# Kernel tuning notes

Measured on AMD Instinct MI355X. Metric: run time of the kernel, lower is better.

## Reference

```python
import jax, jax.numpy as jnp
import numpy as np

EPS = 1e-5
FH, FW, OC = 1, 9, 32  # filt_h, filt_w, out_channels (hardcoded in HypER)


def _bn(x, g, b, axes):
    # training-mode batchnorm: biased variance over `axes`
    m = jnp.mean(x, axis=axes, keepdims=True)
    v = jnp.mean(jnp.square(x - m), axis=axes, keepdims=True)
    return (x - m) * jax.lax.rsqrt(v + EPS) * g + b


def setup_inputs() -> dict:
    key = jax.random.key(0)
    ks = jax.random.split(key, 8)
    N, INPUT_D, D1, D2, B = 50000, 400, 400, 400, 8192
    fc_len = OC * (D1 - FW + 1)  # 32*392 = 12544
    return {
        "head_tail_id": jax.random.randint(ks[0], (2, B), 0, N, dtype=jnp.int32),
        "unique_entity_embed": jax.random.normal(ks[1], (N, INPUT_D), jnp.float32),
        "W_E": jax.random.normal(ks[2], (INPUT_D, D1), jnp.float32) * 0.05,
        "fc1_w": jax.random.normal(ks[3], (OC * FW, D2), jnp.float32) * 0.05,
        "fc1_b": jnp.zeros((OC * FW,), jnp.float32),
        "fc_w": jax.random.normal(ks[4], (D1, fc_len), jnp.float32) * 0.02,
        "fc_b": jnp.zeros((D1,), jnp.float32),
        "bn0_g": jnp.ones((1,), jnp.float32),
        "bn0_b": jnp.zeros((1,), jnp.float32),
        "bn1_g": jnp.ones((OC,), jnp.float32),
        "bn1_b": jnp.zeros((OC,), jnp.float32),
        "bn2_g": jnp.ones((400,), jnp.float32),
        "bn2_b": jnp.zeros((400,), jnp.float32),
    }


def reference(head_tail_id, unique_entity_embed, W_E, fc1_w, fc1_b, fc_w, fc_b,
              bn0_g, bn0_b, bn1_g, bn1_b, bn2_g, bn2_b):
    E = unique_entity_embed @ W_E                    # (N, d1)
    head = E[head_tail_id[0]]                        # (B, d1)
    tail = E[head_tail_id[1]]                        # (B, d1)
    # bn0: BatchNorm2d with 1 channel -> normalize over all B*1*d1 elements
    x = _bn(head, bn0_g[0], bn0_b[0], axes=(0, 1))   # (B, d1)
    # hypernetwork: per-sample dynamic 1x9 filters for 32 out-channels
    k = (tail @ fc1_w.T + fc1_b).reshape(-1, OC, FW)  # (B, 32, 9)
    W_out = x.shape[1] - FW + 1                       # d1-8 = 392
    win_idx = jnp.arange(W_out)[:, None] + jnp.arange(FW)[None, :]
    xw = x[:, win_idx]                                # (B, W_out, 9) sliding windows
    # grouped conv (groups=B), cross-correlation as in F.conv2d
    conv = jnp.einsum('bjw,bow->boj', xw, k)          # (B, 32, W_out)
    # bn1: per out-channel over (B, W_out)
    conv = _bn(conv, bn1_g[None, :, None], bn1_b[None, :, None], axes=(0, 2))
    feat = conv.reshape(conv.shape[0], -1)            # (B, 32*W_out), channel-major flatten
    out = feat @ fc_w.T + fc_b                        # (B, d1)
    out = _bn(out, bn2_g, bn2_b, axes=(0,))           # BatchNorm1d over batch
    return jax.nn.relu(out)
```

## Files before the change

kernel.cpp:

```cpp
#include <hip/hip_runtime.h>


#define BB   8192
#define DD   400
#define RR   288
#define OCC  32
#define FWW  9
#define JJ   392
#define FCLEN 12544
#define KSPL 4
#define KS   (FCLEN / KSPL)
#define KSTEPS (KS / 64)
#define EPSF 1e-5
#define RB2  512

typedef __attribute__((ext_vector_type(8))) short bf16x8;
typedef __attribute__((ext_vector_type(4))) float f32x4;

__device__ inline unsigned short f2bf(float f) {
    union { float f; unsigned u; } x; x.f = f;
    unsigned r = x.u + 0x7fffu + ((x.u >> 16) & 1u);
    return (unsigned short)(r >> 16);
}

__device__ inline void gload16(const void* g, void* l) {
    __builtin_amdgcn_global_load_lds((const __attribute__((address_space(1))) unsigned int*)g,
                                     (__attribute__((address_space(3))) unsigned int*)l, 16, 0, 0);
}

__device__ inline float block_reduce_256(float v, float* red) {
    #pragma unroll
    for (int m = 1; m < 64; m <<= 1) v += __shfl_xor(v, m);
    int wv = threadIdx.x >> 6;
    if ((threadIdx.x & 63) == 0) red[wv] = v;
    __syncthreads();
    float r = 0.f;
    if (threadIdx.x == 0) r = red[0] + red[1] + red[2] + red[3];
    return r;
}

__global__ __launch_bounds__(256) void prep_M(const float* __restrict__ WE,
                                              const float* __restrict__ f1w,
                                              float* __restrict__ Mout) {
    __shared__ float sA[16][17];
    __shared__ float sB[16][17];
    int tx = threadIdx.x, ty = threadIdx.y;
    int r0 = blockIdx.x * 16, i0 = blockIdx.y * 16;
    float acc = 0.f;
    for (int d0 = 0; d0 < DD; d0 += 16) {
        sA[ty][tx] = WE[(size_t)(i0 + ty) * DD + d0 + tx];
        sB[ty][tx] = f1w[(size_t)(r0 + ty) * DD + d0 + tx];
        __syncthreads();
        #pragma unroll
        for (int dd = 0; dd < 16; ++dd) acc = fmaf(sA[ty][dd], sB[tx][dd], acc);
        __syncthreads();
    }
    Mout[(size_t)(i0 + ty) * RR + r0 + tx] = acc;
}

template <int BN>
__global__ __launch_bounds__(256) void gemm_s1(const float* __restrict__ A,
                                               const int* __restrict__ idx,
                                               const float* __restrict__ Bm,
                                               const float* __restrict__ bias,
                                               float* __restrict__ C, int N,
                                               float* __restrict__ bn0part) {
    constexpr int BNF = BN / 16;
    constexpr int BCH = 64 * (BN / 4) / 256;
    __shared__ unsigned short Al[64][72];
    __shared__ unsigned short Bl[BN][72];
    __shared__ int ridx[64];
    __shared__ float red[8];
    int tid = threadIdx.x;
    int bm = blockIdx.x, bn = blockIdx.y;
    if (tid < 64) ridx[tid] = idx[bm * 64 + tid];
    int lane = tid & 63, wv = tid >> 6;
    int m16 = lane & 15, kb = lane >> 4;
    f32x4 acc[BNF];
    #pragma unroll
    for (int nb = 0; nb < BNF; ++nb) acc[nb] = (f32x4){0.f, 0.f, 0.f, 0.f};
    __syncthreads();

    float4 av[4];
    float4 bv[BCH];
    auto LOADR = [&](int k0) {
        #pragma unroll
        for (int r = 0; r < 4; ++r) {
            int c = tid + 256 * r;
            int row = c >> 4, kq = c & 15;
            int gk = k0 + kq * 4;
            av[r] = (float4){0.f, 0.f, 0.f, 0.f};
            if (gk < DD) av[r] = *(const float4*)(A + (size_t)ridx[row] * DD + gk);
        }
        #pragma unroll
        for (int r = 0; r < BCH; ++r) {
            int c = tid + 256 * r;
            int kk2 = c / (BN / 4), nq = c % (BN / 4);
            int gk = k0 + kk2;
            bv[r] = (float4){0.f, 0.f, 0.f, 0.f};
            if (gk < DD) bv[r] = *(const float4*)(Bm + (size_t)gk * N + bn * BN + nq * 4);
        }
    };
    auto WRITELDS = [&]() {
        #pragma unroll
        for (int r = 0; r < 4; ++r) {
            int c = tid + 256 * r;
            int row = c >> 4, kq = c & 15;
            ushort4 p;
            p.x = f2bf(av[r].x); p.y = f2bf(av[r].y); p.z = f2bf(av[r].z); p.w = f2bf(av[r].w);
            *(ushort4*)&Al[row][kq * 4] = p;
        }
        #pragma unroll
        for (int r = 0; r < BCH; ++r) {
            int c = tid + 256 * r;
            int kk2 = c / (BN / 4), nq = c % (BN / 4);
            Bl[nq * 4 + 0][kk2] = f2bf(bv[r].x);
            Bl[nq * 4 + 1][kk2] = f2bf(bv[r].y);
            Bl[nq * 4 + 2][kk2] = f2bf(bv[r].z);
            Bl[nq * 4 + 3][kk2] = f2bf(bv[r].w);
        }
    };

    LOADR(0);
    for (int kt = 0; kt < 7; ++kt) {
        WRITELDS();
        __syncthreads();
        if (kt + 1 < 7) LOADR((kt + 1) * 64);
        #pragma unroll
        for (int ks = 0; ks < 2; ++ks) {
            bf16x8 a = *(const bf16x8*)&Al[wv * 16 + m16][ks * 32 + kb * 8];
            #pragma unroll
            for (int nb = 0; nb < BNF; ++nb) {
                bf16x8 b = *(const bf16x8*)&Bl[nb * 16 + m16][ks * 32 + kb * 8];
                acc[nb] = __builtin_amdgcn_mfma_f32_16x16x32_bf16(a, b, acc[nb], 0, 0, 0);
            }
        }
        __syncthreads();
    }
    float s1 = 0.f, s2 = 0.f;
    #pragma unroll
    for (int nb = 0; nb < BNF; ++nb)
        #pragma unroll
        for (int rr = 0; rr < 4; ++rr) {
            int gr = bm * 64 + wv * 16 + kb * 4 + rr;
            int gc = bn * BN + nb * 16 + m16;
            float v = acc[nb][rr];
            if (bias) v += bias[gc];
            C[(size_t)gr * N + gc] = v;
            s1 += v; s2 = fmaf(v, v, s2);
        }
    if (bn0part) {
        float t1 = block_reduce_256(s1, red);
        __syncthreads();
        float t2 = block_reduce_256(s2, red);
        if (tid == 0) {
            int pid = bm * gridDim.y + bn;
            bn0part[pid * 2] = t1; bn0part[pid * 2 + 1] = t2;
        }
    }
}

__global__ __launch_bounds__(256) void bn0_fin(const float* __restrict__ part,
                                               const float* __restrict__ g,
                                               const float* __restrict__ b,
                                               float* __restrict__ ab0) {
    __shared__ float red[8];
    float s1 = 0.f, s2 = 0.f;
    for (int i = threadIdx.x; i < 640; i += 256) {
        s1 += part[i * 2]; s2 += part[i * 2 + 1];
    }
    float t1 = block_reduce_256(s1, red);
    __syncthreads();
    float t2 = block_reduce_256(s2, red);
    if (threadIdx.x == 0) {
        double n = (double)BB * DD;
        double mean = (double)t1 / n;
        double var = (double)t2 / n - mean * mean;
        float a0 = (float)((double)g[0] / sqrt(var + EPSF));
        float b0 = (float)((double)b[0] - mean * a0);
        ab0[0] = a0; ab0[1] = b0;
    }
}

__global__ __launch_bounds__(256) void conv_k(const float* __restrict__ head,
                                              const float* __restrict__ kbuf,
                                              const float* __restrict__ ab0,
                                              unsigned short* __restrict__ convb,
                                              float* __restrict__ chpartT) {
    __shared__ float xs[DD];
    __shared__ float ks[RR];
    int b = blockIdx.x, tid = threadIdx.x;
    float a0 = ab0[0], b0 = ab0[1];
    for (int i = tid; i < DD; i += 256) xs[i] = fmaf(head[(size_t)b * DD + i], a0, b0);
    for (int i = tid; i < RR; i += 256) ks[i] = kbuf[(size_t)b * RR + i];
    __syncthreads();
    int lane = tid & 63, wv = tid >> 6;
    unsigned short* orow = convb + (size_t)b * FCLEN;
    float kk[8][FWW];
    #pragma unroll
    for (int oi = 0; oi < 8; ++oi)
        #pragma unroll
        for (int w2 = 0; w2 < FWW; ++w2) kk[oi][w2] = ks[(wv * 8 + oi) * FWW + w2];
    float s1[8], s2[8];
    #pragma unroll
    for (int oi = 0; oi < 8; ++oi) { s1[oi] = 0.f; s2[oi] = 0.f; }
    #pragma unroll
    for (int jt = 0; jt < 2; ++jt) {
        int j0 = jt * 256 + lane * 4;
        if (j0 < JJ) {
            const float4* x4 = (const float4*)xs;
            float4 va = x4[(j0 >> 2)], vb = x4[(j0 >> 2) + 1], vc = x4[(j0 >> 2) + 2];
            float x[12] = {va.x, va.y, va.z, va.w, vb.x, vb.y, vb.z, vb.w, vc.x, vc.y, vc.z, vc.w};
            #pragma unroll
            for (int oi = 0; oi < 8; ++oi) {
                float acc[4];
                #pragma unroll
                for (int q = 0; q < 4; ++q) {
                    float a = 0.f;
                    #pragma unroll
                    for (int w2 = 0; w2 < FWW; ++w2) a = fmaf(x[q + w2], kk[oi][w2], a);
                    acc[q] = a;
                }
                ushort4 p;
                p.x = f2bf(acc[0]); p.y = f2bf(acc[1]); p.z = f2bf(acc[2]); p.w = f2bf(acc[3]);
                *(ushort4*)(orow + (wv * 8 + oi) * JJ + j0) = p;
                #pragma unroll
                for (int q = 0; q < 4; ++q) { s1[oi] += acc[q]; s2[oi] = fmaf(acc[q], acc[q], s2[oi]); }
            }
        }
    }
    #pragma unroll
    for (int oi = 0; oi < 8; ++oi) {
        float a = s1[oi], c = s2[oi];
        #pragma unroll
        for (int m = 1; m < 64; m <<= 1) { a += __shfl_xor(a, m); c += __shfl_xor(c, m); }
        if (lane == 0) {
            int o = wv * 8 + oi;
            chpartT[(size_t)o * BB + b] = a;
            chpartT[(size_t)(OCC + o) * BB + b] = c;
        }
    }
}

__global__ __launch_bounds__(256) void bn1_fin(const float* __restrict__ chpartT,
                                               const float* __restrict__ g1,
                                               const float* __restrict__ b1,
                                               float* __restrict__ alphabeta) {
    __shared__ float red[8];
    int o = blockIdx.x, tid = threadIdx.x;
    float s1 = 0.f, s2 = 0.f;
    for (int t = tid; t < BB; t += 256) {
        s1 += chpartT[(size_t)o * BB + t];
        s2 += chpartT[(size_t)(OCC + o) * BB + t];
    }
    float t1 = block_reduce_256(s1, red);
    __syncthreads();
    float t2 = block_reduce_256(s2, red);
    if (tid == 0) {
        double n = (double)BB * JJ;
        double mean = (double)t1 / n;
        double var = (double)t2 / n - mean * mean;
        float al = (float)((double)g1[o] / sqrt(var + EPSF));
        float be = (float)((double)b1[o] - mean * al);
        alphabeta[o] = al; alphabeta[OCC + o] = be;
    }
}

__global__ __launch_bounds__(256) void prep_fcw(const float* __restrict__ fc_w,
                                                const float* __restrict__ fc_b,
                                                const float* __restrict__ alphabeta,
                                                unsigned short* __restrict__ Bp,
                                                float* __restrict__ bias2) {
    __shared__ float al[OCC], be[OCC];
    __shared__ float red[8];
    int d = blockIdx.x, tid = threadIdx.x;
    if (tid < OCC) { al[tid] = alphabeta[tid]; be[tid] = alphabeta[OCC + tid]; }
    __syncthreads();
    const float* row = fc_w + (size_t)d * FCLEN;
    unsigned short* orow = Bp + (size_t)d * FCLEN;
    float bacc = 0.f;
    for (int o = 0; o < OCC; ++o) {
        float a = al[o], bb = be[o];
        for (int j = tid; j < JJ; j += 256) {
            float wv = row[o * JJ + j];
            orow[o * JJ + j] = f2bf(wv * a);
            bacc = fmaf(wv, bb, bacc);
        }
    }
    float t = block_reduce_256(bacc, red);
    if (tid == 0) bias2[d] = fc_b[d] + t;
}

__global__ __launch_bounds__(256, 3) void fc_gemm_sk(const unsigned short* __restrict__ A,
                                                     const unsigned short* __restrict__ Bp,
                                                     float* __restrict__ P) {
    __shared__ __align__(16) unsigned short Al[256 * 64];
    __shared__ __align__(16) unsigned short Bl[80 * 64];
    int tid = threadIdx.x;
    int orig = blockIdx.x;
    int wgid = (orig & 7) * 80 + (orig >> 3);
    int bn = wgid % 5;
    int rest = wgid / 5;
    int bm = rest & 31;
    int bz = rest >> 5;
    int lane = tid & 63, wv = tid >> 6;
    int m16 = lane & 15, kb = lane >> 4;
    int srow = lane >> 3, scol = lane & 7;
    int sw = m16 & 7;
    f32x4 acc[4][5];
    #pragma unroll
    for (int mi = 0; mi < 4; ++mi)
        #pragma unroll
        for (int nb = 0; nb < 5; ++nb) acc[mi][nb] = (f32x4){0.f, 0.f, 0.f, 0.f};

    const unsigned short* Asrc = A + (size_t)(bm * 256 + srow) * FCLEN
                                   + (size_t)bz * KS + ((scol ^ srow) << 3);
    const unsigned short* Bsrc = Bp + (size_t)(bn * 80 + srow) * FCLEN
                                   + (size_t)bz * KS + ((scol ^ srow) << 3);

    for (int kt = 0; kt < KSTEPS; ++kt) {
        const size_t koff = (size_t)kt * 64;
        #pragma unroll
        for (int i = 0; i < 11; ++i) {
            int c = wv + i * 4;
            if (c < 32) {
                gload16(Asrc + (size_t)c * 8 * FCLEN + koff, Al + c * 512);
            } else if (c < 42) {
                int cb = c - 32;
                gload16(Bsrc + (size_t)cb * 8 * FCLEN + koff, Bl + cb * 512);
            }
        }
        __syncthreads();
        #pragma unroll
        for (int ks2 = 0; ks2 < 2; ++ks2) {
            int ch = (((ks2 * 4 + kb) ^ sw) << 3);
            bf16x8 a[4];
            #pragma unroll
            for (int mi = 0; mi < 4; ++mi)
                a[mi] = *(const bf16x8*)(Al + (wv * 64 + mi * 16 + m16) * 64 + ch);
            #pragma unroll
            for (int nb = 0; nb < 5; ++nb) {
                bf16x8 b = *(const bf16x8*)(Bl + (nb * 16 + m16) * 64 + ch);
                #pragma unroll
                for (int mi = 0; mi < 4; ++mi)
                    acc[mi][nb] = __builtin_amdgcn_mfma_f32_16x16x32_bf16(a[mi], b, acc[mi][nb], 0, 0, 0);
            }
        }
        __syncthreads();
    }

    float* Po = P + (size_t)bz * BB * DD;
    #pragma unroll
    for (int mi = 0; mi < 4; ++mi)
        #pragma unroll
        for (int nb = 0; nb < 5; ++nb)
            #pragma unroll
            for (int rr = 0; rr < 4; ++rr) {
                int gr = bm * 256 + wv * 64 + mi * 16 + kb * 4 + rr;
                int gc = bn * 80 + nb * 16 + m16;
                Po[(size_t)gr * DD + gc] = acc[mi][nb][rr];
            }
}

__global__ __launch_bounds__(256) void reduce_bn2(const float* __restrict__ P,
                                                  const float* __restrict__ bias2,
                                                  float* __restrict__ out,
                                                  float* __restrict__ part) {
    int blk = blockIdx.x, tid = threadIdx.x;
    int r0 = blk * 16;
    const size_t S = (size_t)BB * DD;
    bool hasb = tid < DD - 256;
    float bia = bias2[tid];
    float bib = hasb ? bias2[256 + tid] : 0.f;
    float s1a = 0.f, s2a = 0.f, s1b = 0.f, s2b = 0.f;
    for (int r = 0; r < 16; ++r) {
        size_t base = (size_t)(r0 + r) * DD;
        float v = P[base + tid] + P[S + base + tid] + P[2 * S + base + tid] + P[3 * S + base + tid] + bia;
        out[base + tid] = v;
        s1a += v; s2a = fmaf(v, v, s2a);
        if (hasb) {
            size_t b2i = base + 256 + tid;
            float u = P[b2i] + P[S + b2i] + P[2 * S + b2i] + P[3 * S + b2i] + bib;
            out[b2i] = u;
            s1b += u; s2b = fmaf(u, u, s2b);
        }
    }
    float* p = part + (size_t)blk * (DD * 2);
    p[tid * 2] = s1a; p[tid * 2 + 1] = s2a;
    if (hasb) { p[(256 + tid) * 2] = s1b; p[(256 + tid) * 2 + 1] = s2b; }
}

__global__ __launch_bounds__(128) void bn2_fin(const float* __restrict__ part,
                                               const float* __restrict__ g2,
                                               const float* __restrict__ b2,
                                               float* __restrict__ sc,
                                               float* __restrict__ sh) {
    __shared__ float red[4];
    int col = blockIdx.x, tid = threadIdx.x;
    float s1 = 0.f, s2 = 0.f;
    for (int t = tid; t < RB2; t += 128) {
        s1 += part[(size_t)t * (DD * 2) + col * 2];
        s2 += part[(size_t)t * (DD * 2) + col * 2 + 1];
    }
    #pragma unroll
    for (int m = 1; m < 64; m <<= 1) { s1 += __shfl_xor(s1, m); s2 += __shfl_xor(s2, m); }
    int wv = tid >> 6;
    if ((tid & 63) == 0) { red[wv] = s1; red[2 + wv] = s2; }
    __syncthreads();
    if (tid == 0) {
        double t1 = (double)red[0] + red[1];
        double t2 = (double)red[2] + red[3];
        double mean = t1 / (double)BB;
        double var = t2 / (double)BB - mean * mean;
        float s = (float)((double)g2[col] / sqrt(var + EPSF));
        sc[col] = s;
        sh[col] = (float)((double)b2[col] - mean * s);
    }
}

__global__ __launch_bounds__(256) void final_k(float* __restrict__ out,
                                               const float* __restrict__ sc,
                                               const float* __restrict__ sh) {
    __shared__ float lsc[DD], lsh[DD];
    int tid = threadIdx.x;
    for (int c = tid; c < DD; c += 256) { lsc[c] = sc[c]; lsh[c] = sh[c]; }
    __syncthreads();
    size_t base = (size_t)blockIdx.x * 4 * DD;
    for (int r = 0; r < 4; ++r)
        for (int c = tid; c < DD; c += 256) {
            size_t i = base + (size_t)r * DD + c;
            float v = fmaf(out[i], lsc[c], lsh[c]);
            out[i] = v > 0.f ? v : 0.f;
        }
}

extern "C" void kernel_launch(void* const* d_in, const int* in_sizes, int n_in,
                              void* d_out, int out_size, void* d_ws, size_t ws_size,
                              hipStream_t stream) {
    const int* ht      = (const int*)d_in[0];
    const float* UE    = (const float*)d_in[1];
    const float* W_E   = (const float*)d_in[2];
    const float* fc1_w = (const float*)d_in[3];
    const float* fc1_b = (const float*)d_in[4];
    const float* fc_w  = (const float*)d_in[5];
    const float* fc_b  = (const float*)d_in[6];
    const float* bn0_g = (const float*)d_in[7];
    const float* bn0_b = (const float*)d_in[8];
    const float* bn1_g = (const float*)d_in[9];
    const float* bn1_b = (const float*)d_in[10];
    const float* bn2_g = (const float*)d_in[11];
    const float* bn2_b = (const float*)d_in[12];
    float* out = (float*)d_out;

    char* w = (char*)d_ws;
    unsigned short* convb = (unsigned short*)w; w += (size_t)BB * FCLEN * 2;
    unsigned short* Bprep = (unsigned short*)w; w += (size_t)DD * FCLEN * 2;
    float* chpartT = (float*)w; w += (size_t)2 * OCC * BB * 4;
    float* bn0p = (float*)w;  w += 640 * 2 * 4;
    float* ab0 = (float*)w;   w += 64;
    float* alphabeta = (float*)w; w += 64 * 4;
    float* bias2 = (float*)w; w += DD * 4;
    float* bn2p = (float*)w;  w += (size_t)RB2 * DD * 2 * 4;
    float* bn2sc = (float*)w; w += DD * 4;
    float* bn2sh = (float*)w; w += DD * 4;
    float* P = (float*)w;     w += (size_t)KSPL * BB * DD * 4;
    float* head = P;
    float* kbuf = head + (size_t)BB * DD;
    float* Mbuf = kbuf + (size_t)BB * RR;
    (void)ws_size; (void)in_sizes; (void)n_in; (void)out_size;

    prep_M<<<dim3(RR / 16, DD / 16), dim3(16, 16), 0, stream>>>(W_E, fc1_w, Mbuf);
    gemm_s1<80><<<dim3(BB / 64, DD / 80), 256, 0, stream>>>(UE, ht, W_E, nullptr, head, DD, bn0p);
    gemm_s1<96><<<dim3(BB / 64, RR / 96), 256, 0, stream>>>(UE, ht + BB, Mbuf, fc1_b, kbuf, RR, nullptr);
    bn0_fin<<<1, 256, 0, stream>>>(bn0p, bn0_g, bn0_b, ab0);
    conv_k<<<BB, 256, 0, stream>>>(head, kbuf, ab0, convb, chpartT);
    bn1_fin<<<OCC, 256, 0, stream>>>(chpartT, bn1_g, bn1_b, alphabeta);
    prep_fcw<<<DD, 256, 0, stream>>>(fc_w, fc_b, alphabeta, Bprep, bias2);
    fc_gemm_sk<<<dim3(32 * 5 * KSPL), 256, 0, stream>>>(convb, Bprep, P);
    reduce_bn2<<<RB2, 256, 0, stream>>>(P, bias2, out, bn2p);
    bn2_fin<<<DD, 128, 0, stream>>>(bn2p, bn2_g, bn2_b, bn2sc, bn2sh);
    final_k<<<2048, 256, 0, stream>>>(out, bn2sc, bn2sh);
}
```

Before: 336.1 us.

## Fuse bn0 finalize into conv, nontemporal conv stores, vectorize prep_fcw and final_k

Removes the single-block bn0_fin kernel by having every conv_k block redundantly reduce the 640 bn0 partials and compute the scale and shift itself, applying them to the loaded row in registers. Conv output stores become nontemporal 8-byte stores, prep_fcw is rewritten to read fc_w as float4 and write packed bf16x4, and final_k processes 8 rows per block with float4 accesses. The aim is to save a launch, cut cache pollution from the large conv buffer and raise memory efficiency. The cost is 8192 blocks each re-reading and reducing the partials.

```diff
diff --git a/kernel.cpp b/kernel.cpp
--- a/kernel.cpp
+++ b/kernel.cpp
@@ -1,4 +1,5 @@
 #include <hip/hip_runtime.h>
+#include <string.h>
 
 
 #define BB   8192
@@ -16,6 +17,7 @@
 
 typedef __attribute__((ext_vector_type(8))) short bf16x8;
 typedef __attribute__((ext_vector_type(4))) float f32x4;
+typedef __attribute__((ext_vector_type(2))) unsigned int u32x2;
 
 __device__ inline unsigned short f2bf(float f) {
     union { float f; unsigned u; } x; x.f = f;
@@ -26,6 +28,12 @@
 __device__ inline void gload16(const void* g, void* l) {
     __builtin_amdgcn_global_load_lds((const __attribute__((address_space(1))) unsigned int*)g,
                                      (__attribute__((address_space(3))) unsigned int*)l, 16, 0, 0);
+}
+
+__device__ inline void nt_store8(void* addr, ushort4 v) {
+    u32x2 w;
+    memcpy(&w, &v, 8);
+    __builtin_nontemporal_store(w, (u32x2*)addr);
 }
 
 __device__ inline float block_reduce_256(float v, float* red) {
@@ -160,40 +168,34 @@
     }
 }
 
-__global__ __launch_bounds__(256) void bn0_fin(const float* __restrict__ part,
-                                               const float* __restrict__ g,
-                                               const float* __restrict__ b,
-                                               float* __restrict__ ab0) {
-    __shared__ float red[8];
-    float s1 = 0.f, s2 = 0.f;
-    for (int i = threadIdx.x; i < 640; i += 256) {
-        s1 += part[i * 2]; s2 += part[i * 2 + 1];
-    }
-    float t1 = block_reduce_256(s1, red);
-    __syncthreads();
-    float t2 = block_reduce_256(s2, red);
-    if (threadIdx.x == 0) {
-        double n = (double)BB * DD;
-        double mean = (double)t1 / n;
-        double var = (double)t2 / n - mean * mean;
-        float a0 = (float)((double)g[0] / sqrt(var + EPSF));
-        float b0 = (float)((double)b[0] - mean * a0);
-        ab0[0] = a0; ab0[1] = b0;
-    }
-}
-
 __global__ __launch_bounds__(256) void conv_k(const float* __restrict__ head,
                                               const float* __restrict__ kbuf,
-                                              const float* __restrict__ ab0,
+                                              const float* __restrict__ bn0p,
+                                              const float* __restrict__ g0,
+                                              const float* __restrict__ b0g,
                                               unsigned short* __restrict__ convb,
                                               float* __restrict__ chpartT) {
     __shared__ float xs[DD];
     __shared__ float ks[RR];
+    __shared__ float red[8];
+    __shared__ float ab[2];
     int b = blockIdx.x, tid = threadIdx.x;
-    float a0 = ab0[0], b0 = ab0[1];
-    for (int i = tid; i < DD; i += 256) xs[i] = fmaf(head[(size_t)b * DD + i], a0, b0);
+    for (int i = tid; i < DD; i += 256) xs[i] = head[(size_t)b * DD + i];
     for (int i = tid; i < RR; i += 256) ks[i] = kbuf[(size_t)b * RR + i];
-    __syncthreads();
+    float p1 = 0.f, p2 = 0.f;
+    for (int i = tid; i < 640; i += 256) { p1 += bn0p[i * 2]; p2 += bn0p[i * 2 + 1]; }
+    float t1 = block_reduce_256(p1, red);
+    __syncthreads();
+    float t2 = block_reduce_256(p2, red);
+    if (tid == 0) {
+        double n = (double)BB * DD;
+        double mean = (double)t1 / n;
+        double var = (double)t2 / n - mean * mean;
+        float a0 = (float)((double)g0[0] / sqrt(var + EPSF));
+        ab[0] = a0; ab[1] = (float)((double)b0g[0] - mean * a0);
+    }
+    __syncthreads();
+    float a0 = ab[0], b0 = ab[1];
     int lane = tid & 63, wv = tid >> 6;
     unsigned short* orow = convb + (size_t)b * FCLEN;
     float kk[8][FWW];
@@ -210,7 +212,10 @@
         if (j0 < JJ) {
             const float4* x4 = (const float4*)xs;
             float4 va = x4[(j0 >> 2)], vb = x4[(j0 >> 2) + 1], vc = x4[(j0 >> 2) + 2];
-            float x[12] = {va.x, va.y, va.z, va.w, vb.x, vb.y, vb.z, vb.w, vc.x, vc.y, vc.z, vc.w};
+            float xr[12] = {va.x, va.y, va.z, va.w, vb.x, vb.y, vb.z, vb.w, vc.x, vc.y, vc.z, vc.w};
+            float x[12];
+            #pragma unroll
+            for (int q = 0; q < 12; ++q) x[q] = fmaf(xr[q], a0, b0);
             #pragma unroll
             for (int oi = 0; oi < 8; ++oi) {
                 float acc[4];
@@ -223,7 +228,7 @@
                 }
                 ushort4 p;
                 p.x = f2bf(acc[0]); p.y = f2bf(acc[1]); p.z = f2bf(acc[2]); p.w = f2bf(acc[3]);
-                *(ushort4*)(orow + (wv * 8 + oi) * JJ + j0) = p;
+                nt_store8(orow + (wv * 8 + oi) * JJ + j0, p);
                 #pragma unroll
                 for (int q = 0; q < 4; ++q) { s1[oi] += acc[q]; s2[oi] = fmaf(acc[q], acc[q], s2[oi]); }
             }
@@ -276,16 +281,18 @@
     int d = blockIdx.x, tid = threadIdx.x;
     if (tid < OCC) { al[tid] = alphabeta[tid]; be[tid] = alphabeta[OCC + tid]; }
     __syncthreads();
-    const float* row = fc_w + (size_t)d * FCLEN;
-    unsigned short* orow = Bp + (size_t)d * FCLEN;
+    const float4* row4 = (const float4*)(fc_w + (size_t)d * FCLEN);
+    ushort4* orow4 = (ushort4*)(Bp + (size_t)d * FCLEN);
     float bacc = 0.f;
-    for (int o = 0; o < OCC; ++o) {
+    for (int c = tid; c < FCLEN / 4; c += 256) {
+        float4 v = row4[c];
+        int o = c / (JJ / 4);
         float a = al[o], bb = be[o];
-        for (int j = tid; j < JJ; j += 256) {
-            float wv = row[o * JJ + j];
-            orow[o * JJ + j] = f2bf(wv * a);
-            bacc = fmaf(wv, bb, bacc);
-        }
+        ushort4 p;
+        p.x = f2bf(v.x * a); p.y = f2bf(v.y * a);
+        p.z = f2bf(v.z * a); p.w = f2bf(v.w * a);
+        orow4[c] = p;
+        bacc = fmaf(v.x + v.y + v.z + v.w, bb, bacc);
     }
     float t = block_reduce_256(bacc, red);
     if (tid == 0) bias2[d] = fc_b[d] + t;
@@ -425,13 +432,18 @@
     int tid = threadIdx.x;
     for (int c = tid; c < DD; c += 256) { lsc[c] = sc[c]; lsh[c] = sh[c]; }
     __syncthreads();
-    size_t base = (size_t)blockIdx.x * 4 * DD;
-    for (int r = 0; r < 4; ++r)
-        for (int c = tid; c < DD; c += 256) {
-            size_t i = base + (size_t)r * DD + c;
-            float v = fmaf(out[i], lsc[c], lsh[c]);
-            out[i] = v > 0.f ? v : 0.f;
-        }
+    int r0 = blockIdx.x * 8;
+    float4* out4 = (float4*)(out + (size_t)r0 * DD);
+    for (int c = tid; c < 8 * DD / 4; c += 256) {
+        int row = c / (DD / 4), c4 = c % (DD / 4);
+        float4 v = out4[(size_t)row * (DD / 4) + c4];
+        int cb = c4 * 4;
+        v.x = fmaf(v.x, lsc[cb + 0], lsh[cb + 0]); v.x = v.x > 0.f ? v.x : 0.f;
+        v.y = fmaf(v.y, lsc[cb + 1], lsh[cb + 1]); v.y = v.y > 0.f ? v.y : 0.f;
+        v.z = fmaf(v.z, lsc[cb + 2], lsh[cb + 2]); v.z = v.z > 0.f ? v.z : 0.f;
+        v.w = fmaf(v.w, lsc[cb + 3], lsh[cb + 3]); v.w = v.w > 0.f ? v.w : 0.f;
+        out4[(size_t)row * (DD / 4) + c4] = v;
+    }
 }
 
 extern "C" void kernel_launch(void* const* d_in, const int* in_sizes, int n_in,
@@ -457,7 +469,6 @@
     unsigned short* Bprep = (unsigned short*)w; w += (size_t)DD * FCLEN * 2;
     float* chpartT = (float*)w; w += (size_t)2 * OCC * BB * 4;
     float* bn0p = (float*)w;  w += 640 * 2 * 4;
-    float* ab0 = (float*)w;   w += 64;
     float* alphabeta = (float*)w; w += 64 * 4;
     float* bias2 = (float*)w; w += DD * 4;
     float* bn2p = (float*)w;  w += (size_t)RB2 * DD * 2 * 4;
@@ -472,12 +483,11 @@
     prep_M<<<dim3(RR / 16, DD / 16), dim3(16, 16), 0, stream>>>(W_E, fc1_w, Mbuf);
     gemm_s1<80><<<dim3(BB / 64, DD / 80), 256, 0, stream>>>(UE, ht, W_E, nullptr, head, DD, bn0p);
     gemm_s1<96><<<dim3(BB / 64, RR / 96), 256, 0, stream>>>(UE, ht + BB, Mbuf, fc1_b, kbuf, RR, nullptr);
-    bn0_fin<<<1, 256, 0, stream>>>(bn0p, bn0_g, bn0_b, ab0);
-    conv_k<<<BB, 256, 0, stream>>>(head, kbuf, ab0, convb, chpartT);
+    conv_k<<<BB, 256, 0, stream>>>(head, kbuf, bn0p, bn0_g, bn0_b, convb, chpartT);
     bn1_fin<<<OCC, 256, 0, stream>>>(chpartT, bn1_g, bn1_b, alphabeta);
     prep_fcw<<<DD, 256, 0, stream>>>(fc_w, fc_b, alphabeta, Bprep, bias2);
     fc_gemm_sk<<<dim3(32 * 5 * KSPL), 256, 0, stream>>>(convb, Bprep, P);
     reduce_bn2<<<RB2, 256, 0, stream>>>(P, bias2, out, bn2p);
     bn2_fin<<<DD, 128, 0, stream>>>(bn2p, bn2_g, bn2_b, bn2sc, bn2sh);
-    final_k<<<2048, 256, 0, stream>>>(out, bn2sc, bn2sh);
-}
+    final_k<<<BB / 8, 256, 0, stream>>>(out, bn2sc, bn2sh);
+}
```

After: 314.7 us. 6.4% less time.
